# Optimization experiments

Hardware: AMD Instinct MI355X
Metric: run time of the kernel (lower is better)

## Reference

```python
import jax, jax.numpy as jnp
import numpy as np

NUM_EMBEDDINGS = 8192
EMBEDDING_DIM = 512
COMMITMENT_COST = 0.25
N_INPUTS = 32768


def setup_inputs() -> dict:
    key = jax.random.key(0)
    k1, k2 = jax.random.split(key)
    inputs = jax.random.normal(k1, (N_INPUTS, EMBEDDING_DIM), dtype=jnp.float32)
    weight = jax.random.normal(k2, (NUM_EMBEDDINGS, EMBEDDING_DIM), dtype=jnp.float32)
    return {"inputs": inputs, "weight": weight}


def reference(inputs, weight):
    # distances[n, k] = ||x_n||^2 + ||w_k||^2 - 2 x_n . w_k   -> [N, K]
    distances = (
        jnp.sum(inputs ** 2, axis=1, keepdims=True)
        + jnp.sum(weight ** 2, axis=1)
        - 2.0 * (inputs @ weight.T)
    )
    probs = jax.nn.softmax(-distances, axis=-1)            # [N, K]
    idx = jnp.argmin(distances, axis=1)                    # [N]
    quantized = weight[idx]                                # gather == one-hot @ weight

    e_latent_loss = jnp.mean((jax.lax.stop_gradient(quantized) - inputs) ** 2)
    q_latent_loss = jnp.mean((quantized - jax.lax.stop_gradient(inputs)) ** 2)
    loss = q_latent_loss + COMMITMENT_COST * e_latent_loss

    # straight-through estimator
    quantized_st = inputs + jax.lax.stop_gradient(quantized - inputs)

    # avg over one-hot encodings == normalized code histogram
    counts = jnp.bincount(idx, length=NUM_EMBEDDINGS).astype(inputs.dtype)
    avg_probs = counts / inputs.shape[0]
    perplexity = jnp.exp(-jnp.sum(avg_probs * jnp.log(avg_probs + 1e-10)))

    return (quantized_st, probs, loss, perplexity)
```

## Files before the change

kernel.cpp:

```cpp
#include <hip/hip_runtime.h>
#include <hip/hip_fp16.h>
#include <math.h>

#define N_ROWS 32768
#define K_CODES 8192
#define DIM 512

#define OUT_Q 0
#define OUT_P ((size_t)N_ROWS * DIM)
#define OUT_LOSS (OUT_P + (size_t)N_ROWS * K_CODES)
#define OUT_PERP (OUT_LOSS + 1)

#define WS_XSQ 0
#define WS_WSQ (N_ROWS)
#define WS_LOSS (N_ROWS + K_CODES)
#define WS_CNT (WS_LOSS + 1)
#define WS_F16 51200

#define XH_OFF ((size_t)0)
#define XL_OFF ((size_t)N_ROWS * DIM)
#define WH_OFF ((size_t)2 * N_ROWS * DIM)
#define WL_OFF ((size_t)2 * N_ROWS * DIM + (size_t)K_CODES * DIM)
#define F16_COUNT ((size_t)2 * (N_ROWS + K_CODES) * DIM)
#define WS_NEEDED ((size_t)WS_F16 * 4 + F16_COUNT * 2)

typedef _Float16 f16x8 __attribute__((ext_vector_type(8)));
typedef float f32x4 __attribute__((ext_vector_type(4)));

__device__ inline void load_lds16(const void* g, void* l) {
    __builtin_amdgcn_global_load_lds((const __attribute__((address_space(1))) void*)g,
                                     (__attribute__((address_space(3))) void*)l,
                                     16, 0, 0);
}

__global__ void sq_norms_kernel(const float* __restrict__ X,
                                const float* __restrict__ W,
                                float* __restrict__ ws) {
    int row = blockIdx.x;
    int lane = threadIdx.x;
    const float* src;
    float* dst;
    if (row < N_ROWS) {
        src = X + (size_t)row * DIM;
        dst = ws + WS_XSQ + row;
    } else {
        src = W + (size_t)(row - N_ROWS) * DIM;
        dst = ws + WS_WSQ + (row - N_ROWS);
    }
    float4 v0 = *(const float4*)(src + lane * 8);
    float4 v1 = *(const float4*)(src + lane * 8 + 4);
    float s = v0.x * v0.x + v0.y * v0.y + v0.z * v0.z + v0.w * v0.w
            + v1.x * v1.x + v1.y * v1.y + v1.z * v1.z + v1.w * v1.w;
#pragma unroll
    for (int off = 32; off > 0; off >>= 1) s += __shfl_down(s, off, 64);
    if (lane == 0) *dst = s;
}

__global__ void __launch_bounds__(256) convert_split_kernel(
    const float* __restrict__ X, const float* __restrict__ W,
    _Float16* __restrict__ f16base) {
    const size_t NX8 = (size_t)N_ROWS * DIM / 8;
    size_t t = (size_t)blockIdx.x * 256 + threadIdx.x;
    const float* src;
    _Float16 *hd, *ld;
    if (t < NX8) {
        src = X + t * 8;
        hd = f16base + XH_OFF + t * 8;
        ld = f16base + XL_OFF + t * 8;
    } else {
        size_t u = t - NX8;
        src = W + u * 8;
        hd = f16base + WH_OFF + u * 8;
        ld = f16base + WL_OFF + u * 8;
    }
    float4 v0 = *(const float4*)src;
    float4 v1 = *(const float4*)(src + 4);
    float v[8] = {v0.x, v0.y, v0.z, v0.w, v1.x, v1.y, v1.z, v1.w};
    f16x8 h, l;
#pragma unroll
    for (int i = 0; i < 8; ++i) {
        _Float16 hv = (_Float16)v[i];
        h[i] = hv;
        l[i] = (_Float16)(v[i] - (float)hv);
    }
    *(f16x8*)hd = h;
    *(f16x8*)ld = l;
}

__global__ void __launch_bounds__(256) gemm_dist_mfma_kernel(
    const _Float16* __restrict__ f16base, const float* __restrict__ ws,
    float* __restrict__ out) {
    __shared__ _Float16 lds[4][128][32];

    const int tid = threadIdx.x;
    const int w = tid >> 6;
    const int lane = tid & 63;
    const int bn = blockIdx.x * 128;
    const int bm = blockIdx.y * 128;
    const int wr = w >> 1;
    const int wc = w & 1;

    const _Float16* src_base;
    int tile_row_base;
    if (w == 0)      { src_base = f16base + XH_OFF; tile_row_base = bm; }
    else if (w == 1) { src_base = f16base + XL_OFF; tile_row_base = bm; }
    else if (w == 2) { src_base = f16base + WH_OFF; tile_row_base = bn; }
    else             { src_base = f16base + WL_OFF; tile_row_base = bn; }

    const int lrow = lane >> 2;
    const int p = lane & 3;

    f32x4 acc[4][4];
#pragma unroll
    for (int i = 0; i < 4; ++i)
#pragma unroll
        for (int j = 0; j < 4; ++j) acc[i][j] = (f32x4){0.f, 0.f, 0.f, 0.f};

    const int q = lane >> 4;
    const int fm = lane & 15;

    for (int k0 = 0; k0 < DIM; k0 += 32) {
        __syncthreads();
#pragma unroll
        for (int e = 0; e < 8; ++e) {
            int m = e * 16 + lrow;
            int c = p ^ ((m >> 1) & 3);
            const _Float16* gp =
                src_base + (size_t)(tile_row_base + m) * DIM + k0 + c * 8;
            load_lds16(gp, &lds[w][e * 16][0]);
        }
        __syncthreads();

        f16x8 ah[4], al[4], bh[4], bl[4];
#pragma unroll
        for (int i = 0; i < 4; ++i) {
            int am = wr * 64 + i * 16 + fm;
            int sa = (am >> 1) & 3;
            ah[i] = *(const f16x8*)&lds[0][am][(q ^ sa) * 8];
            al[i] = *(const f16x8*)&lds[1][am][(q ^ sa) * 8];
            int bb = wc * 64 + i * 16 + fm;
            int sb = (bb >> 1) & 3;
            bh[i] = *(const f16x8*)&lds[2][bb][(q ^ sb) * 8];
            bl[i] = *(const f16x8*)&lds[3][bb][(q ^ sb) * 8];
        }
#pragma unroll
        for (int i = 0; i < 4; ++i)
#pragma unroll
            for (int j = 0; j < 4; ++j) {
                acc[i][j] = __builtin_amdgcn_mfma_f32_16x16x32_f16(
                    ah[i], bh[j], acc[i][j], 0, 0, 0);
                acc[i][j] = __builtin_amdgcn_mfma_f32_16x16x32_f16(
                    ah[i], bl[j], acc[i][j], 0, 0, 0);
                acc[i][j] = __builtin_amdgcn_mfma_f32_16x16x32_f16(
                    al[i], bh[j], acc[i][j], 0, 0, 0);
            }
    }

    const float* xsq = ws + WS_XSQ;
    const float* wsq = ws + WS_WSQ;
    float* Dout = out + OUT_P;
    const int q4 = (lane >> 4) * 4;
#pragma unroll
    for (int i = 0; i < 4; ++i) {
#pragma unroll
        for (int j = 0; j < 4; ++j) {
            int n = bn + wc * 64 + j * 16 + fm;
            float wn = wsq[n];
#pragma unroll
            for (int r = 0; r < 4; ++r) {
                int m = bm + wr * 64 + i * 16 + q4 + r;
                Dout[(size_t)m * K_CODES + n] = xsq[m] + wn - 2.f * acc[i][j][r];
            }
        }
    }
}

#define BM 128
#define BN 128
#define BK 16

__global__ void __launch_bounds__(256) gemm_dist_fp32_kernel(
    const float* __restrict__ X, const float* __restrict__ W,
    const float* __restrict__ ws, float* __restrict__ out) {
    __shared__ float As[BK][BM];
    __shared__ float Bs[BK][BN];

    const int bn = blockIdx.x * BN;
    const int bm = blockIdx.y * BM;
    const int tid = threadIdx.x;
    const int tx = tid & 15;
    const int ty = tid >> 4;
    const int lr = tid >> 1;
    const int lc = (tid & 1) * 8;

    float acc[8][8];
#pragma unroll
    for (int i = 0; i < 8; ++i)
#pragma unroll
        for (int j = 0; j < 8; ++j) acc[i][j] = 0.f;

    const float* aptr = X + (size_t)(bm + lr) * DIM + lc;
    const float* bptr = W + (size_t)(bn + lr) * DIM + lc;

    for (int k0 = 0; k0 < DIM; k0 += BK) {
        float4 a0 = *(const float4*)(aptr + k0);
        float4 a1 = *(const float4*)(aptr + k0 + 4);
        float4 b0 = *(const float4*)(bptr + k0);
        float4 b1 = *(const float4*)(bptr + k0 + 4);
        __syncthreads();
        As[lc + 0][lr] = a0.x; As[lc + 1][lr] = a0.y;
        As[lc + 2][lr] = a0.z; As[lc + 3][lr] = a0.w;
        As[lc + 4][lr] = a1.x; As[lc + 5][lr] = a1.y;
        As[lc + 6][lr] = a1.z; As[lc + 7][lr] = a1.w;
        Bs[lc + 0][lr] = b0.x; Bs[lc + 1][lr] = b0.y;
        Bs[lc + 2][lr] = b0.z; Bs[lc + 3][lr] = b0.w;
        Bs[lc + 4][lr] = b1.x; Bs[lc + 5][lr] = b1.y;
        Bs[lc + 6][lr] = b1.z; Bs[lc + 7][lr] = b1.w;
        __syncthreads();
#pragma unroll
        for (int kk = 0; kk < BK; ++kk) {
            float a[8], b[8];
            *(float4*)&a[0] = *(const float4*)&As[kk][ty * 8];
            *(float4*)&a[4] = *(const float4*)&As[kk][ty * 8 + 4];
            *(float4*)&b[0] = *(const float4*)&Bs[kk][tx * 8];
            *(float4*)&b[4] = *(const float4*)&Bs[kk][tx * 8 + 4];
#pragma unroll
            for (int i = 0; i < 8; ++i)
#pragma unroll
                for (int j = 0; j < 8; ++j)
                    acc[i][j] = fmaf(a[i], b[j], acc[i][j]);
        }
    }

    const float* xsq = ws + WS_XSQ;
    const float* wsq = ws + WS_WSQ;
    const int m0 = bm + ty * 8;
    const int n0 = bn + tx * 8;
    float wn[8];
    *(float4*)&wn[0] = *(const float4*)(wsq + n0);
    *(float4*)&wn[4] = *(const float4*)(wsq + n0 + 4);
    float* Dout = out + OUT_P;
#pragma unroll
    for (int i = 0; i < 8; ++i) {
        float xv = xsq[m0 + i];
        float4 o0, o1;
        o0.x = xv + wn[0] - 2.f * acc[i][0];
        o0.y = xv + wn[1] - 2.f * acc[i][1];
        o0.z = xv + wn[2] - 2.f * acc[i][2];
        o0.w = xv + wn[3] - 2.f * acc[i][3];
        o1.x = xv + wn[4] - 2.f * acc[i][4];
        o1.y = xv + wn[5] - 2.f * acc[i][5];
        o1.z = xv + wn[6] - 2.f * acc[i][6];
        o1.w = xv + wn[7] - 2.f * acc[i][7];
        float* drow = Dout + (size_t)(m0 + i) * K_CODES + n0;
        *(float4*)(drow) = o0;
        *(float4*)(drow + 4) = o1;
    }
}

__global__ void __launch_bounds__(256) row_softmax_kernel(
    const float* __restrict__ X, const float* __restrict__ W,
    float* __restrict__ out, float* __restrict__ ws) {
    const int n = blockIdx.x;
    const int tid = threadIdx.x;
    __shared__ float sD[K_CODES];
    __shared__ float red_v[256];
    __shared__ int red_i[256];

    float* Drow = out + OUT_P + (size_t)n * K_CODES;

    float4* sD4 = (float4*)sD;
    for (int i = tid; i < K_CODES / 4; i += 256) {
        sD4[i] = *(const float4*)(Drow + i * 4);
    }
    __syncthreads();

    float bv = INFINITY;
    int bi = 0x7fffffff;
    for (int j = tid; j < K_CODES; j += 256) {
        float v = sD[j];
        if (v < bv || (v == bv && j < bi)) { bv = v; bi = j; }
    }
    red_v[tid] = bv;
    red_i[tid] = bi;
    __syncthreads();
    for (int s = 128; s > 0; s >>= 1) {
        if (tid < s) {
            float ov = red_v[tid + s];
            int oi = red_i[tid + s];
            if (ov < red_v[tid] || (ov == red_v[tid] && oi < red_i[tid])) {
                red_v[tid] = ov;
                red_i[tid] = oi;
            }
        }
        __syncthreads();
    }
    const float dmin = red_v[0];
    const int amin = red_i[0];
    __syncthreads();

    float s = 0.f;
    for (int j = tid; j < K_CODES; j += 256) {
        float e = __expf(dmin - sD[j]);
        sD[j] = e;
        s += e;
    }
    red_v[tid] = s;
    __syncthreads();
    for (int st = 128; st > 0; st >>= 1) {
        if (tid < st) red_v[tid] += red_v[tid + st];
        __syncthreads();
    }
    const float inv = 1.0f / red_v[0];
    __syncthreads();

    for (int i = tid; i < K_CODES / 4; i += 256) {
        float4 e = sD4[i];
        float4 p;
        p.x = e.x * inv; p.y = e.y * inv; p.z = e.z * inv; p.w = e.w * inv;
        *(float4*)(Drow + i * 4) = p;
    }

    const float* wrow = W + (size_t)amin * DIM;
    const float* xrow = X + (size_t)n * DIM;
    float* qrow = out + OUT_Q + (size_t)n * DIM;
    float errs = 0.f;
    for (int c = tid; c < DIM; c += 256) {
        float x = xrow[c];
        float qv = wrow[c];
        float d = qv - x;
        qrow[c] = x + d;
        errs += d * d;
    }
    red_v[tid] = errs;
    __syncthreads();
    for (int st = 128; st > 0; st >>= 1) {
        if (tid < st) red_v[tid] += red_v[tid + st];
        __syncthreads();
    }
    if (tid == 0) {
        atomicAdd(ws + WS_LOSS, red_v[0]);
        atomicAdd(ws + WS_CNT + amin, 1.0f);
    }
}

__global__ void __launch_bounds__(256) finalize_kernel(
    float* __restrict__ out, const float* __restrict__ ws) {
    __shared__ float red[256];
    const int tid = threadIdx.x;
    float ent = 0.f;
    for (int j = tid; j < K_CODES; j += 256) {
        float p = ws[WS_CNT + j] * (1.0f / (float)N_ROWS);
        ent -= p * logf(p + 1e-10f);
    }
    red[tid] = ent;
    __syncthreads();
    for (int st = 128; st > 0; st >>= 1) {
        if (tid < st) red[tid] += red[tid + st];
        __syncthreads();
    }
    if (tid == 0) {
        float mse = ws[WS_LOSS] * (1.0f / ((float)N_ROWS * (float)DIM));
        out[OUT_LOSS] = mse + 0.25f * mse;
        out[OUT_PERP] = expf(red[0]);
    }
}

extern "C" void kernel_launch(void* const* d_in, const int* in_sizes, int n_in,
                              void* d_out, int out_size, void* d_ws, size_t ws_size,
                              hipStream_t stream) {
    const float* X = (const float*)d_in[0];
    const float* W = (const float*)d_in[1];
    float* out = (float*)d_out;
    float* ws = (float*)d_ws;

    hipMemsetAsync(ws + WS_LOSS, 0, (1 + K_CODES) * sizeof(float), stream);

    sq_norms_kernel<<<N_ROWS + K_CODES, 64, 0, stream>>>(X, W, ws);

    if (ws_size >= WS_NEEDED) {
        _Float16* f16base = (_Float16*)(ws + WS_F16);
        const int conv_blocks = (int)(((size_t)(N_ROWS + K_CODES) * DIM / 8 + 255) / 256);
        convert_split_kernel<<<conv_blocks, 256, 0, stream>>>(X, W, f16base);

        dim3 ggrid(K_CODES / 128, N_ROWS / 128);
        gemm_dist_mfma_kernel<<<ggrid, 256, 0, stream>>>(f16base, ws, out);
    } else {
        dim3 ggrid(K_CODES / BN, N_ROWS / BM);
        gemm_dist_fp32_kernel<<<ggrid, 256, 0, stream>>>(X, W, ws, out);
    }

    row_softmax_kernel<<<N_ROWS, 256, 0, stream>>>(X, W, out, ws);

    finalize_kernel<<<1, 256, 0, stream>>>(out, ws);
}
```

Before: 2.444 ms.

## Fuse row argmin into GEMM epilogue and drop row-norm term from distances

The GEMM epilogue now packs each distance with its column index into a 64-bit key, reduces it across lanes and atomically mins it into a per-row table, so the row argmin is computed during the GEMM. The ||x||^2 term is removed from the stored distances because it is constant per row and cancels in both softmax and argmin, which also removes the X-norm kernel. The old LDS-based row softmax is replaced by a register-resident probs kernel that only does exp, sum and normalise, plus a separate small quantisation and loss kernel. In exchange the epilogue gains 64-bit atomics, and the fp16 split precision now also decides which code is chosen by argmin.

```diff
diff --git a/kernel.cpp b/kernel.cpp
--- a/kernel.cpp
+++ b/kernel.cpp
@@ -11,11 +11,11 @@
 #define OUT_LOSS (OUT_P + (size_t)N_ROWS * K_CODES)
 #define OUT_PERP (OUT_LOSS + 1)
 
-#define WS_XSQ 0
-#define WS_WSQ (N_ROWS)
-#define WS_LOSS (N_ROWS + K_CODES)
-#define WS_CNT (WS_LOSS + 1)
-#define WS_F16 51200
+#define WS_WSQ 0
+#define WS_LOSS (K_CODES)
+#define WS_CNT (K_CODES + 1)
+#define WS_ROWTAB 16386
+#define WS_F16 81928
 
 #define XH_OFF ((size_t)0)
 #define XL_OFF ((size_t)N_ROWS * DIM)
@@ -23,6 +23,7 @@
 #define WL_OFF ((size_t)2 * N_ROWS * DIM + (size_t)K_CODES * DIM)
 #define F16_COUNT ((size_t)2 * (N_ROWS + K_CODES) * DIM)
 #define WS_NEEDED ((size_t)WS_F16 * 4 + F16_COUNT * 2)
+#define WS_NEEDED_FALLBACK ((size_t)WS_F16 * 4)
 
 typedef _Float16 f16x8 __attribute__((ext_vector_type(8)));
 typedef float f32x4 __attribute__((ext_vector_type(4)));
@@ -33,27 +34,26 @@
                                      16, 0, 0);
 }
 
-__global__ void sq_norms_kernel(const float* __restrict__ X,
-                                const float* __restrict__ W,
-                                float* __restrict__ ws) {
+__device__ inline unsigned int fkey(float f) {
+    unsigned int b = __float_as_uint(f);
+    return b ^ ((unsigned int)((int)b >> 31) | 0x80000000u);
+}
+__device__ inline float fkey_inv(unsigned int k) {
+    unsigned int b = (k & 0x80000000u) ? (k ^ 0x80000000u) : ~k;
+    return __uint_as_float(b);
+}
+
+__global__ void wsq_kernel(const float* __restrict__ W, float* __restrict__ ws) {
     int row = blockIdx.x;
     int lane = threadIdx.x;
-    const float* src;
-    float* dst;
-    if (row < N_ROWS) {
-        src = X + (size_t)row * DIM;
-        dst = ws + WS_XSQ + row;
-    } else {
-        src = W + (size_t)(row - N_ROWS) * DIM;
-        dst = ws + WS_WSQ + (row - N_ROWS);
-    }
+    const float* src = W + (size_t)row * DIM;
     float4 v0 = *(const float4*)(src + lane * 8);
     float4 v1 = *(const float4*)(src + lane * 8 + 4);
     float s = v0.x * v0.x + v0.y * v0.y + v0.z * v0.z + v0.w * v0.w
             + v1.x * v1.x + v1.y * v1.y + v1.z * v1.z + v1.w * v1.w;
 #pragma unroll
     for (int off = 32; off > 0; off >>= 1) s += __shfl_down(s, off, 64);
-    if (lane == 0) *dst = s;
+    if (lane == 0) ws[WS_WSQ + row] = s;
 }
 
 __global__ void __launch_bounds__(256) convert_split_kernel(
@@ -88,7 +88,7 @@
 }
 
 __global__ void __launch_bounds__(256) gemm_dist_mfma_kernel(
-    const _Float16* __restrict__ f16base, const float* __restrict__ ws,
+    const _Float16* __restrict__ f16base, float* __restrict__ ws,
     float* __restrict__ out) {
     __shared__ _Float16 lds[4][128][32];
 
@@ -156,12 +156,13 @@
             }
     }
 
-    const float* xsq = ws + WS_XSQ;
     const float* wsq = ws + WS_WSQ;
+    unsigned long long* rowtab = (unsigned long long*)(ws + WS_ROWTAB);
     float* Dout = out + OUT_P;
     const int q4 = (lane >> 4) * 4;
 #pragma unroll
     for (int i = 0; i < 4; ++i) {
+        unsigned long long best[4] = {~0ull, ~0ull, ~0ull, ~0ull};
 #pragma unroll
         for (int j = 0; j < 4; ++j) {
             int n = bn + wc * 64 + j * 16 + fm;
@@ -169,7 +170,24 @@
 #pragma unroll
             for (int r = 0; r < 4; ++r) {
                 int m = bm + wr * 64 + i * 16 + q4 + r;
-                Dout[(size_t)m * K_CODES + n] = xsq[m] + wn - 2.f * acc[i][j][r];
+                float s = wn - 2.f * acc[i][j][r];
+                Dout[(size_t)m * K_CODES + n] = s;
+                unsigned long long pk =
+                    ((unsigned long long)fkey(s) << 32) | (unsigned int)n;
+                best[r] = pk < best[r] ? pk : best[r];
+            }
+        }
+#pragma unroll
+        for (int r = 0; r < 4; ++r) {
+            unsigned long long b = best[r];
+#pragma unroll
+            for (int d = 1; d < 16; d <<= 1) {
+                unsigned long long o = __shfl_xor(b, d, 64);
+                b = o < b ? o : b;
+            }
+            if (fm == 0) {
+                int m = bm + wr * 64 + i * 16 + q4 + r;
+                atomicMin(rowtab + m, b);
             }
         }
     }
@@ -232,7 +250,6 @@
         }
     }
 
-    const float* xsq = ws + WS_XSQ;
     const float* wsq = ws + WS_WSQ;
     const int m0 = bm + ty * 8;
     const int n0 = bn + tx * 8;
@@ -242,104 +259,112 @@
     float* Dout = out + OUT_P;
 #pragma unroll
     for (int i = 0; i < 8; ++i) {
-        float xv = xsq[m0 + i];
         float4 o0, o1;
-        o0.x = xv + wn[0] - 2.f * acc[i][0];
-        o0.y = xv + wn[1] - 2.f * acc[i][1];
-        o0.z = xv + wn[2] - 2.f * acc[i][2];
-        o0.w = xv + wn[3] - 2.f * acc[i][3];
-        o1.x = xv + wn[4] - 2.f * acc[i][4];
-        o1.y = xv + wn[5] - 2.f * acc[i][5];
-        o1.z = xv + wn[6] - 2.f * acc[i][6];
-        o1.w = xv + wn[7] - 2.f * acc[i][7];
+        o0.x = wn[0] - 2.f * acc[i][0];
+        o0.y = wn[1] - 2.f * acc[i][1];
+        o0.z = wn[2] - 2.f * acc[i][2];
+        o0.w = wn[3] - 2.f * acc[i][3];
+        o1.x = wn[4] - 2.f * acc[i][4];
+        o1.y = wn[5] - 2.f * acc[i][5];
+        o1.z = wn[6] - 2.f * acc[i][6];
+        o1.w = wn[7] - 2.f * acc[i][7];
         float* drow = Dout + (size_t)(m0 + i) * K_CODES + n0;
         *(float4*)(drow) = o0;
         *(float4*)(drow + 4) = o1;
     }
 }
 
-__global__ void __launch_bounds__(256) row_softmax_kernel(
+__global__ void __launch_bounds__(256) rowmin_scan_kernel(
+    const float* __restrict__ out, float* __restrict__ ws) {
+    const int n = blockIdx.x;
+    const int tid = threadIdx.x;
+    const float* Drow = out + OUT_P + (size_t)n * K_CODES;
+    unsigned long long b = ~0ull;
+    for (int j = tid; j < K_CODES; j += 256) {
+        unsigned long long pk =
+            ((unsigned long long)fkey(Drow[j]) << 32) | (unsigned int)j;
+        b = pk < b ? pk : b;
+    }
+#pragma unroll
+    for (int d = 1; d < 64; d <<= 1) {
+        unsigned long long o = __shfl_xor(b, d, 64);
+        b = o < b ? o : b;
+    }
+    __shared__ unsigned long long wmin[4];
+    if ((tid & 63) == 0) wmin[tid >> 6] = b;
+    __syncthreads();
+    if (tid == 0) {
+        unsigned long long m = wmin[0];
+        m = wmin[1] < m ? wmin[1] : m;
+        m = wmin[2] < m ? wmin[2] : m;
+        m = wmin[3] < m ? wmin[3] : m;
+        ((unsigned long long*)(ws + WS_ROWTAB))[n] = m;
+    }
+}
+
+__global__ void __launch_bounds__(256) probs_kernel(
+    float* __restrict__ out, const float* __restrict__ ws) {
+    const int n = blockIdx.x;
+    const int tid = threadIdx.x;
+    const unsigned long long tab =
+        ((const unsigned long long*)(ws + WS_ROWTAB))[n];
+    const float smin = fkey_inv((unsigned int)(tab >> 32));
+
+    float4* Drow = (float4*)(out + OUT_P + (size_t)n * K_CODES);
+    float4 e[8];
+    float sum = 0.f;
+#pragma unroll
+    for (int t = 0; t < 8; ++t) {
+        float4 v = Drow[tid + t * 256];
+        float4 ev;
+        ev.x = __expf(smin - v.x);
+        ev.y = __expf(smin - v.y);
+        ev.z = __expf(smin - v.z);
+        ev.w = __expf(smin - v.w);
+        e[t] = ev;
+        sum += ev.x + ev.y + ev.z + ev.w;
+    }
+#pragma unroll
+    for (int off = 32; off > 0; off >>= 1) sum += __shfl_down(sum, off, 64);
+    __shared__ float wsum[4];
+    if ((tid & 63) == 0) wsum[tid >> 6] = sum;
+    __syncthreads();
+    const float inv = 1.0f / (wsum[0] + wsum[1] + wsum[2] + wsum[3]);
+#pragma unroll
+    for (int t = 0; t < 8; ++t) {
+        float4 ev = e[t];
+        ev.x *= inv; ev.y *= inv; ev.z *= inv; ev.w *= inv;
+        Drow[tid + t * 256] = ev;
+    }
+}
+
+__global__ void __launch_bounds__(64) quant_loss_kernel(
     const float* __restrict__ X, const float* __restrict__ W,
     float* __restrict__ out, float* __restrict__ ws) {
     const int n = blockIdx.x;
-    const int tid = threadIdx.x;
-    __shared__ float sD[K_CODES];
-    __shared__ float red_v[256];
-    __shared__ int red_i[256];
-
-    float* Drow = out + OUT_P + (size_t)n * K_CODES;
-
-    float4* sD4 = (float4*)sD;
-    for (int i = tid; i < K_CODES / 4; i += 256) {
-        sD4[i] = *(const float4*)(Drow + i * 4);
-    }
-    __syncthreads();
-
-    float bv = INFINITY;
-    int bi = 0x7fffffff;
-    for (int j = tid; j < K_CODES; j += 256) {
-        float v = sD[j];
-        if (v < bv || (v == bv && j < bi)) { bv = v; bi = j; }
-    }
-    red_v[tid] = bv;
-    red_i[tid] = bi;
-    __syncthreads();
-    for (int s = 128; s > 0; s >>= 1) {
-        if (tid < s) {
-            float ov = red_v[tid + s];
-            int oi = red_i[tid + s];
-            if (ov < red_v[tid] || (ov == red_v[tid] && oi < red_i[tid])) {
-                red_v[tid] = ov;
-                red_i[tid] = oi;
-            }
-        }
-        __syncthreads();
-    }
-    const float dmin = red_v[0];
-    const int amin = red_i[0];
-    __syncthreads();
-
-    float s = 0.f;
-    for (int j = tid; j < K_CODES; j += 256) {
-        float e = __expf(dmin - sD[j]);
-        sD[j] = e;
-        s += e;
-    }
-    red_v[tid] = s;
-    __syncthreads();
-    for (int st = 128; st > 0; st >>= 1) {
-        if (tid < st) red_v[tid] += red_v[tid + st];
-        __syncthreads();
-    }
-    const float inv = 1.0f / red_v[0];
-    __syncthreads();
-
-    for (int i = tid; i < K_CODES / 4; i += 256) {
-        float4 e = sD4[i];
-        float4 p;
-        p.x = e.x * inv; p.y = e.y * inv; p.z = e.z * inv; p.w = e.w * inv;
-        *(float4*)(Drow + i * 4) = p;
-    }
-
-    const float* wrow = W + (size_t)amin * DIM;
-    const float* xrow = X + (size_t)n * DIM;
-    float* qrow = out + OUT_Q + (size_t)n * DIM;
-    float errs = 0.f;
-    for (int c = tid; c < DIM; c += 256) {
-        float x = xrow[c];
-        float qv = wrow[c];
-        float d = qv - x;
-        qrow[c] = x + d;
-        errs += d * d;
-    }
-    red_v[tid] = errs;
-    __syncthreads();
-    for (int st = 128; st > 0; st >>= 1) {
-        if (tid < st) red_v[tid] += red_v[tid + st];
-        __syncthreads();
-    }
-    if (tid == 0) {
-        atomicAdd(ws + WS_LOSS, red_v[0]);
+    const int lane = threadIdx.x;
+    const unsigned long long tab =
+        ((const unsigned long long*)(ws + WS_ROWTAB))[n];
+    const int amin = (int)(tab & 0xFFFFFFFFu);
+
+    const float4* xr = (const float4*)(X + (size_t)n * DIM);
+    const float4* wr = (const float4*)(W + (size_t)amin * DIM);
+    float4* qr = (float4*)(out + OUT_Q + (size_t)n * DIM);
+    float err = 0.f;
+#pragma unroll
+    for (int t = 0; t < 2; ++t) {
+        float4 x = xr[lane + t * 64];
+        float4 qv = wr[lane + t * 64];
+        float4 d, o;
+        d.x = qv.x - x.x; d.y = qv.y - x.y; d.z = qv.z - x.z; d.w = qv.w - x.w;
+        o.x = x.x + d.x;  o.y = x.y + d.y;  o.z = x.z + d.z;  o.w = x.w + d.w;
+        qr[lane + t * 64] = o;
+        err += d.x * d.x + d.y * d.y + d.z * d.z + d.w * d.w;
+    }
+#pragma unroll
+    for (int off = 32; off > 0; off >>= 1) err += __shfl_down(err, off, 64);
+    if (lane == 0) {
+        atomicAdd(ws + WS_LOSS, err);
         atomicAdd(ws + WS_CNT + amin, 1.0f);
     }
 }
@@ -375,12 +400,14 @@
     float* ws = (float*)d_ws;
 
     hipMemsetAsync(ws + WS_LOSS, 0, (1 + K_CODES) * sizeof(float), stream);
-
-    sq_norms_kernel<<<N_ROWS + K_CODES, 64, 0, stream>>>(X, W, ws);
+    hipMemsetAsync(ws + WS_ROWTAB, 0xFF, (size_t)N_ROWS * 8, stream);
+
+    wsq_kernel<<<K_CODES, 64, 0, stream>>>(W, ws);
 
     if (ws_size >= WS_NEEDED) {
         _Float16* f16base = (_Float16*)(ws + WS_F16);
-        const int conv_blocks = (int)(((size_t)(N_ROWS + K_CODES) * DIM / 8 + 255) / 256);
+        const int conv_blocks =
+            (int)(((size_t)(N_ROWS + K_CODES) * DIM / 8 + 255) / 256);
         convert_split_kernel<<<conv_blocks, 256, 0, stream>>>(X, W, f16base);
 
         dim3 ggrid(K_CODES / 128, N_ROWS / 128);
@@ -388,9 +415,10 @@
     } else {
         dim3 ggrid(K_CODES / BN, N_ROWS / BM);
         gemm_dist_fp32_kernel<<<ggrid, 256, 0, stream>>>(X, W, ws, out);
-    }
-
-    row_softmax_kernel<<<N_ROWS, 256, 0, stream>>>(X, W, out, ws);
-
+        rowmin_scan_kernel<<<N_ROWS, 256, 0, stream>>>(out, ws);
+    }
+
+    probs_kernel<<<N_ROWS, 256, 0, stream>>>(out, ws);
+    quant_loss_kernel<<<N_ROWS, 64, 0, stream>>>(X, W, out, ws);
     finalize_kernel<<<1, 256, 0, stream>>>(out, ws);
 }
```

New measurement: 3.275 ms. 34.0% more time.
